# Performance work log

Measured on AMD Instinct MI355X. Metric: run time of the kernel, lower is better.

## Reference

```python
import jax, jax.numpy as jnp
import numpy as np

N_NODES = 50000
N_EDGES = 1600000
IN_FEAT = 48
OUT_FEAT = 48
NUM_RELS = 8


def setup_inputs() -> dict:
    key = jax.random.key(0)
    ks = jax.random.split(key, 9)
    # xavier-ish scale for relu gain
    s1 = float(np.sqrt(2.0) * np.sqrt(6.0 / (IN_FEAT + IN_FEAT)))
    s2 = float(np.sqrt(2.0) * np.sqrt(6.0 / (IN_FEAT + OUT_FEAT)))
    return {
        "inputs": jax.random.normal(ks[0], (N_NODES, IN_FEAT), dtype=jnp.float32),
        "norm": jax.random.uniform(ks[1], (N_EDGES, 1), dtype=jnp.float32),
        "weight1": jax.random.uniform(ks[2], (NUM_RELS, IN_FEAT, IN_FEAT), jnp.float32, -s1, s1),
        "weight2": jax.random.uniform(ks[3], (NUM_RELS, IN_FEAT, OUT_FEAT), jnp.float32, -s2, s2),
        "bias1": jax.random.normal(ks[4], (IN_FEAT,), dtype=jnp.float32) * 0.1,
        "bias2": jax.random.normal(ks[5], (OUT_FEAT,), dtype=jnp.float32) * 0.1,
        "src": jax.random.randint(ks[6], (N_EDGES,), 0, N_NODES, dtype=jnp.int64) if jax.config.jax_enable_x64 else jax.random.randint(ks[6], (N_EDGES,), 0, N_NODES).astype(jnp.int32),
        "dst": jax.random.randint(ks[7], (N_EDGES,), 0, N_NODES).astype(jnp.int32),
        "rel_type": jax.random.randint(ks[8], (N_EDGES,), 0, NUM_RELS).astype(jnp.int32),
    }


def reference(inputs, norm, weight1, weight2, bias1, bias2, src, dst, rel_type):
    # Message depends only on (src node, relation): precompute per (node, rel).
    # Stage 1: h1[n,r,:] = relu(h[n] @ W1[r] + b1)   -> [N, R, in]
    h1 = jax.nn.relu(jnp.einsum('ni,rij->nrj', inputs, weight1) + bias1)
    # Stage 2: h2[n,r,:] = h1[n,r] @ W2[r]           -> [N, R, out]
    h2 = jnp.einsum('nrj,rjo->nro', h1, weight2)
    # Per-edge gather + norm scaling                 -> [E, out]
    msg = h2[src, rel_type] * norm
    # Scatter-sum aggregation to destination nodes   -> [N, out]
    agg = jax.ops.segment_sum(msg, dst, num_segments=inputs.shape[0])
    # apply_func: bias2 + activation
    return jax.nn.relu(agg + bias2)
```

## Files before the change

kernel.cpp:

```cpp
#include <hip/hip_runtime.h>

#define NN 50000
#define EE 1600000
#define FF 48
#define RR 8
#define H2R 48
#define LSTR 72
#define NSEG 8
#define SCAP 16

#define WB 8
#define ZB 391
#define K1GRID (WB + ZB)

#define H2TILES 391
#define PB ((EE + 255) / 256)
#define K2GRID (H2TILES + PB)

typedef __attribute__((ext_vector_type(8))) short frag8;
typedef __attribute__((ext_vector_type(4))) float frag4f;
typedef __attribute__((ext_vector_type(4))) unsigned uint4v;

__device__ inline unsigned short bf16r(float f) {
    unsigned u = __float_as_uint(f);
    return (unsigned short)((u + 0x7FFFu + ((u >> 16) & 1u)) >> 16);
}
__device__ inline unsigned bf16pack2(float a, float b) {
    return (unsigned)bf16r(a) | ((unsigned)bf16r(b) << 16);
}
__device__ inline frag8 pack8(float4 a, float4 b) {
    union { frag8 f; unsigned u[4]; } r;
    r.u[0] = bf16pack2(a.x, a.y); r.u[1] = bf16pack2(a.z, a.w);
    r.u[2] = bf16pack2(b.x, b.y); r.u[3] = bf16pack2(b.z, b.w);
    return r.f;
}

__global__ __launch_bounds__(256) void pre_kernel(
    const float* __restrict__ W1, const float* __restrict__ W2,
    unsigned short* __restrict__ W1t, unsigned short* __restrict__ W2t,
    int* __restrict__ count)
{
    int b = blockIdx.x;
    if (b < WB) {
        int r = b;
        const float* w1 = W1 + (size_t)r * FF * FF;
        const float* w2 = W2 + (size_t)r * FF * FF;
        for (int idx = threadIdx.x; idx < 48 * 64; idx += 256) {
            int j = idx >> 6, k = idx & 63;
            W1t[(size_t)r * 48 * 64 + idx] = (k < FF) ? bf16r(w1[k * FF + j]) : (unsigned short)0;
            W2t[(size_t)r * 48 * 64 + idx] = (k < FF) ? bf16r(w2[k * FF + j]) : (unsigned short)0;
        }
        return;
    }
    int z = (b - WB) * 256 + threadIdx.x;
    if (z < 100000) ((int4*)count)[z] = make_int4(0, 0, 0, 0);
}

__global__ __launch_bounds__(256) void h2_place_kernel(
    const float* __restrict__ X, const unsigned short* __restrict__ W1t,
    const unsigned short* __restrict__ W2t, const float* __restrict__ B1,
    const int* __restrict__ srcv, const int* __restrict__ dstv,
    const int* __restrict__ relv, const float* __restrict__ norm,
    int* __restrict__ count, unsigned* __restrict__ payload,
    unsigned short* __restrict__ H2)
{
    __shared__ __align__(16) unsigned short h1s[128 * LSTR];
    __shared__ __align__(16) unsigned short h2s[128 * 96];
    int b = blockIdx.x;
    if (b >= H2TILES) {
        int e = (b - H2TILES) * 256 + threadIdx.x;
        if (e < EE) {
            int xcd;
            asm volatile("s_getreg_b32 %0, hwreg(HW_REG_XCC_ID)" : "=s"(xcd));
            xcd &= (NSEG - 1);
            int d = dstv[e];
            unsigned qn = (unsigned)(norm[e] * 8192.0f + 0.5f);
            if (qn > 8191u) qn = 8191u;
            unsigned rec = ((unsigned)(srcv[e] * 8 + relv[e]) << 13) | qn;
            int x = xcd;
            #pragma unroll 1
            for (int attempt = 0; attempt < NSEG; ++attempt) {
                int pos = atomicAdd(&count[x * NN + d], 1);
                if (pos < SCAP) {
                    payload[((size_t)x * NN + d) * SCAP + pos] = rec;
                    break;
                }
                x = (x + 1) & (NSEG - 1);
            }
        }
        return;
    }
    int tid  = threadIdx.x;
    int w    = tid >> 6, ln = tid & 63, q = ln >> 4, lq = ln & 15;
    int nb   = b * 128 + w * 32;

    unsigned short* myh1 = &h1s[(w * 32) * LSTR];
    unsigned short* myh2 = &h2s[w * 32 * 96];
    for (int i = ln; i < 32 * 12; i += 64) {
        int rr = i / 12, cs = i - rr * 12;
        *(unsigned*)&myh1[rr * LSTR + 48 + cs * 2] = 0;
    }

    int row0 = nb + lq;      if (row0 >= NN) row0 = NN - 1;
    int row1 = nb + 16 + lq; if (row1 >= NN) row1 = NN - 1;
    const float* x0 = X + (size_t)row0 * FF;
    const float* x1 = X + (size_t)row1 * FF;

    frag8 a00 = pack8(*(const float4*)(x0 + q * 8), *(const float4*)(x0 + q * 8 + 4));
    frag8 a10 = pack8(*(const float4*)(x1 + q * 8), *(const float4*)(x1 + q * 8 + 4));
    frag8 a01 = {0, 0, 0, 0, 0, 0, 0, 0};
    frag8 a11 = {0, 0, 0, 0, 0, 0, 0, 0};
    if (q < 2) {
        a01 = pack8(*(const float4*)(x0 + 32 + q * 8), *(const float4*)(x0 + 36 + q * 8));
        a11 = pack8(*(const float4*)(x1 + 32 + q * 8), *(const float4*)(x1 + 36 + q * 8));
    }

    float bcv[3] = {B1[lq], B1[16 + lq], B1[32 + lq]};

    #pragma unroll 1
    for (int kp = 0; kp < 4; ++kp) {
        #pragma unroll
        for (int p = 0; p < 2; ++p) {
            int r = (kp << 1) + p;
            const unsigned short* w1r = W1t + (size_t)r * 48 * 64;
            const unsigned short* w2r = W2t + (size_t)r * 48 * 64;

            #pragma unroll
            for (int t = 0; t < 3; ++t) {
                int col = t * 16 + lq;
                frag8 b0 = *(const frag8*)&w1r[(col << 6) + q * 8];
                frag8 b1 = *(const frag8*)&w1r[(col << 6) + 32 + q * 8];
                float bc = bcv[t];
                frag4f acc0 = {bc, bc, bc, bc};
                frag4f acc1 = {bc, bc, bc, bc};
                acc0 = __builtin_amdgcn_mfma_f32_16x16x32_bf16(a00, b0, acc0, 0, 0, 0);
                acc0 = __builtin_amdgcn_mfma_f32_16x16x32_bf16(a01, b1, acc0, 0, 0, 0);
                acc1 = __builtin_amdgcn_mfma_f32_16x16x32_bf16(a10, b0, acc1, 0, 0, 0);
                acc1 = __builtin_amdgcn_mfma_f32_16x16x32_bf16(a11, b1, acc1, 0, 0, 0);
                #pragma unroll
                for (int g = 0; g < 4; ++g) {
                    myh1[(q * 4 + g) * LSTR + col]      = bf16r(fmaxf(acc0[g], 0.0f));
                    myh1[(16 + q * 4 + g) * LSTR + col] = bf16r(fmaxf(acc1[g], 0.0f));
                }
            }

            const frag8 c00 = *(const frag8*)&myh1[lq * LSTR + q * 8];
            const frag8 c01 = *(const frag8*)&myh1[lq * LSTR + 32 + q * 8];
            const frag8 c10 = *(const frag8*)&myh1[(16 + lq) * LSTR + q * 8];
            const frag8 c11 = *(const frag8*)&myh1[(16 + lq) * LSTR + 32 + q * 8];

            #pragma unroll
            for (int t = 0; t < 3; ++t) {
                int col = t * 16 + lq;
                frag8 b0 = *(const frag8*)&w2r[(col << 6) + q * 8];
                frag8 b1 = *(const frag8*)&w2r[(col << 6) + 32 + q * 8];
                frag4f acc0 = {0.f, 0.f, 0.f, 0.f};
                frag4f acc1 = {0.f, 0.f, 0.f, 0.f};
                acc0 = __builtin_amdgcn_mfma_f32_16x16x32_bf16(c00, b0, acc0, 0, 0, 0);
                acc0 = __builtin_amdgcn_mfma_f32_16x16x32_bf16(c01, b1, acc0, 0, 0, 0);
                acc1 = __builtin_amdgcn_mfma_f32_16x16x32_bf16(c10, b0, acc1, 0, 0, 0);
                acc1 = __builtin_amdgcn_mfma_f32_16x16x32_bf16(c11, b1, acc1, 0, 0, 0);
                #pragma unroll
                for (int g = 0; g < 4; ++g) {
                    myh2[(q * 4 + g) * 96 + p * 48 + col]      = bf16r(acc0[g]);
                    myh2[(16 + q * 4 + g) * 96 + p * 48 + col] = bf16r(acc1[g]);
                }
            }
        }
        #pragma unroll
        for (int i6 = 0; i6 < 6; ++i6) {
            int fl    = i6 * 64 + ln;
            int row   = fl / 12;
            int piece = fl - row * 12;
            int n     = nb + row;
            if (n < NN) {
                uint4v v = *(const uint4v*)&myh2[fl * 8];
                __builtin_nontemporal_store(v,
                    (uint4v*)(H2 + ((size_t)n * RR + kp * 2) * H2R) + piece);
            }
        }
    }
}

__global__ __launch_bounds__(256) void gather_kernel(
    const unsigned short* __restrict__ H2, const unsigned* __restrict__ payload,
    const int* __restrict__ count, const float* __restrict__ B2,
    float* __restrict__ out)
{
    unsigned tid = blockIdx.x * 256u + threadIdx.x;
    unsigned n = tid / 12u;
    unsigned c = tid - n * 12u;
    if (n >= NN) return;

    int cx[NSEG];
    #pragma unroll
    for (int x = 0; x < NSEG; ++x) cx[x] = min(count[(size_t)x * NN + n], SCAP);
    int p1 = cx[0], p2 = p1 + cx[1], p3 = p2 + cx[2], p4 = p3 + cx[3];
    int p5 = p4 + cx[4], p6 = p5 + cx[5], p7 = p6 + cx[6];
    int total = p7 + cx[7];
    const unsigned* pl = payload + (size_t)n * SCAP;

    auto slot = [&](int idx) -> unsigned {
        int x, base;
        if (idx < p4) {
            if (idx < p2) { x = (idx < p1) ? 0 : 1; base = (idx < p1) ? 0 : p1; }
            else          { x = (idx < p3) ? 2 : 3; base = (idx < p3) ? p2 : p3; }
        } else {
            if (idx < p6) { x = (idx < p5) ? 4 : 5; base = (idx < p5) ? p4 : p5; }
            else          { x = (idx < p7) ? 6 : 7; base = (idx < p7) ? p6 : p7; }
        }
        return pl[(size_t)x * (NN * SCAP) + (idx - base)];
    };

    float a0 = 0.f, a1 = 0.f, a2 = 0.f, a3 = 0.f;
    int e = 0;
    for (; e + 8 <= total; e += 8) {
        unsigned p[8];
        #pragma unroll
        for (int k = 0; k < 8; ++k) p[k] = slot(e + k);
        uint2 v[8];
        #pragma unroll
        for (int k = 0; k < 8; ++k)
            v[k] = ((const uint2*)(H2 + (size_t)(p[k] >> 13) * H2R))[c];
        #pragma unroll
        for (int k = 0; k < 8; ++k) {
            float nm = (float)(p[k] & 8191u) * (1.0f / 8192.0f);
            a0 = fmaf(__uint_as_float(v[k].x << 16),         nm, a0);
            a1 = fmaf(__uint_as_float(v[k].x & 0xFFFF0000u), nm, a1);
            a2 = fmaf(__uint_as_float(v[k].y << 16),         nm, a2);
            a3 = fmaf(__uint_as_float(v[k].y & 0xFFFF0000u), nm, a3);
        }
    }
    for (; e < total; ++e) {
        unsigned p = slot(e);
        float nm = (float)(p & 8191u) * (1.0f / 8192.0f);
        uint2 v = ((const uint2*)(H2 + (size_t)(p >> 13) * H2R))[c];
        a0 = fmaf(__uint_as_float(v.x << 16),         nm, a0);
        a1 = fmaf(__uint_as_float(v.x & 0xFFFF0000u), nm, a1);
        a2 = fmaf(__uint_as_float(v.y << 16),         nm, a2);
        a3 = fmaf(__uint_as_float(v.y & 0xFFFF0000u), nm, a3);
    }
    float4 bbb = ((const float4*)B2)[c];
    ((float4*)out)[(size_t)n * 12u + c] = make_float4(
        fmaxf(a0 + bbb.x, 0.f), fmaxf(a1 + bbb.y, 0.f),
        fmaxf(a2 + bbb.z, 0.f), fmaxf(a3 + bbb.w, 0.f));
}

extern "C" void kernel_launch(void* const* d_in, const int* in_sizes, int n_in,
                              void* d_out, int out_size, void* d_ws, size_t ws_size,
                              hipStream_t stream) {
    const float* X   = (const float*)d_in[0];
    const float* nrm = (const float*)d_in[1];
    const float* W1  = (const float*)d_in[2];
    const float* W2  = (const float*)d_in[3];
    const float* B1  = (const float*)d_in[4];
    const float* B2  = (const float*)d_in[5];
    const int*   src = (const int*)d_in[6];
    const int*   dst = (const int*)d_in[7];
    const int*   rel = (const int*)d_in[8];
    float* out = (float*)d_out;

    unsigned short* H2      = (unsigned short*)d_ws;
    unsigned*       payload = (unsigned*)(H2 + (size_t)NN * RR * H2R);
    unsigned short* W1t     = (unsigned short*)(payload + (size_t)NN * NSEG * SCAP);
    unsigned short* W2t     = W1t + RR * 48 * 64;
    int*            count   = (int*)(W2t + RR * 48 * 64);

    pre_kernel<<<K1GRID, 256, 0, stream>>>(W1, W2, W1t, W2t, count);

    h2_place_kernel<<<K2GRID, 256, 0, stream>>>(
        X, W1t, W2t, B1, src, dst, rel, nrm, count, payload, H2);

    unsigned total = (unsigned)NN * 12u;
    gather_kernel<<<(total + 255) / 256, 256, 0, stream>>>(
        H2, payload, count, B2, out);
}
```

Measured before the change: 233.9 us.

## Switch H2 to relation-major layout and drop separate h2 shared buffer

```diff
diff --git a/kernel.cpp b/kernel.cpp
--- a/kernel.cpp
+++ b/kernel.cpp
@@ -20,6 +20,7 @@
 typedef __attribute__((ext_vector_type(8))) short frag8;
 typedef __attribute__((ext_vector_type(4))) float frag4f;
 typedef __attribute__((ext_vector_type(4))) unsigned uint4v;
+typedef __attribute__((ext_vector_type(4))) float float4v;
 
 __device__ inline unsigned short bf16r(float f) {
     unsigned u = __float_as_uint(f);
@@ -28,7 +29,7 @@
 __device__ inline unsigned bf16pack2(float a, float b) {
     return (unsigned)bf16r(a) | ((unsigned)bf16r(b) << 16);
 }
-__device__ inline frag8 pack8(float4 a, float4 b) {
+__device__ inline frag8 pack8(float4v a, float4v b) {
     union { frag8 f; unsigned u[4]; } r;
     r.u[0] = bf16pack2(a.x, a.y); r.u[1] = bf16pack2(a.z, a.w);
     r.u[2] = bf16pack2(b.x, b.y); r.u[3] = bf16pack2(b.z, b.w);
@@ -65,7 +66,6 @@
     unsigned short* __restrict__ H2)
 {
     __shared__ __align__(16) unsigned short h1s[128 * LSTR];
-    __shared__ __align__(16) unsigned short h2s[128 * 96];
     int b = blockIdx.x;
     if (b >= H2TILES) {
         int e = (b - H2TILES) * 256 + threadIdx.x;
@@ -73,10 +73,13 @@
             int xcd;
             asm volatile("s_getreg_b32 %0, hwreg(HW_REG_XCC_ID)" : "=s"(xcd));
             xcd &= (NSEG - 1);
-            int d = dstv[e];
-            unsigned qn = (unsigned)(norm[e] * 8192.0f + 0.5f);
+            int d  = __builtin_nontemporal_load(&dstv[e]);
+            int sv = __builtin_nontemporal_load(&srcv[e]);
+            int rv = __builtin_nontemporal_load(&relv[e]);
+            float nmv = __builtin_nontemporal_load(&norm[e]);
+            unsigned qn = (unsigned)(nmv * 8192.0f + 0.5f);
             if (qn > 8191u) qn = 8191u;
-            unsigned rec = ((unsigned)(srcv[e] * 8 + relv[e]) << 13) | qn;
+            unsigned rec = ((unsigned)(rv * NN + sv) << 13) | qn;
             int x = xcd;
             #pragma unroll 1
             for (int attempt = 0; attempt < NSEG; ++attempt) {
@@ -95,7 +98,6 @@
     int nb   = b * 128 + w * 32;
 
     unsigned short* myh1 = &h1s[(w * 32) * LSTR];
-    unsigned short* myh2 = &h2s[w * 32 * 96];
     for (int i = ln; i < 32 * 12; i += 64) {
         int rr = i / 12, cs = i - rr * 12;
         *(unsigned*)&myh1[rr * LSTR + 48 + cs * 2] = 0;
@@ -103,81 +105,80 @@
 
     int row0 = nb + lq;      if (row0 >= NN) row0 = NN - 1;
     int row1 = nb + 16 + lq; if (row1 >= NN) row1 = NN - 1;
-    const float* x0 = X + (size_t)row0 * FF;
-    const float* x1 = X + (size_t)row1 * FF;
-
-    frag8 a00 = pack8(*(const float4*)(x0 + q * 8), *(const float4*)(x0 + q * 8 + 4));
-    frag8 a10 = pack8(*(const float4*)(x1 + q * 8), *(const float4*)(x1 + q * 8 + 4));
+    const float4v* x0 = (const float4v*)(X + (size_t)row0 * FF);
+    const float4v* x1 = (const float4v*)(X + (size_t)row1 * FF);
+
+    frag8 a00 = pack8(__builtin_nontemporal_load(x0 + q * 2),
+                      __builtin_nontemporal_load(x0 + q * 2 + 1));
+    frag8 a10 = pack8(__builtin_nontemporal_load(x1 + q * 2),
+                      __builtin_nontemporal_load(x1 + q * 2 + 1));
     frag8 a01 = {0, 0, 0, 0, 0, 0, 0, 0};
     frag8 a11 = {0, 0, 0, 0, 0, 0, 0, 0};
     if (q < 2) {
-        a01 = pack8(*(const float4*)(x0 + 32 + q * 8), *(const float4*)(x0 + 36 + q * 8));
-        a11 = pack8(*(const float4*)(x1 + 32 + q * 8), *(const float4*)(x1 + 36 + q * 8));
+        a01 = pack8(__builtin_nontemporal_load(x0 + 8 + q * 2),
+                    __builtin_nontemporal_load(x0 + 9 + q * 2));
+        a11 = pack8(__builtin_nontemporal_load(x1 + 8 + q * 2),
+                    __builtin_nontemporal_load(x1 + 9 + q * 2));
     }
 
     float bcv[3] = {B1[lq], B1[16 + lq], B1[32 + lq]};
 
     #pragma unroll 1
-    for (int kp = 0; kp < 4; ++kp) {
-        #pragma unroll
-        for (int p = 0; p < 2; ++p) {
-            int r = (kp << 1) + p;
-            const unsigned short* w1r = W1t + (size_t)r * 48 * 64;
-            const unsigned short* w2r = W2t + (size_t)r * 48 * 64;
-
+    for (int r = 0; r < RR; ++r) {
+        const unsigned short* w1r = W1t + (size_t)r * 48 * 64;
+        const unsigned short* w2r = W2t + (size_t)r * 48 * 64;
+
+        #pragma unroll
+        for (int t = 0; t < 3; ++t) {
+            int col = t * 16 + lq;
+            frag8 b0 = *(const frag8*)&w1r[(col << 6) + q * 8];
+            frag8 b1 = *(const frag8*)&w1r[(col << 6) + 32 + q * 8];
+            float bc = bcv[t];
+            frag4f acc0 = {bc, bc, bc, bc};
+            frag4f acc1 = {bc, bc, bc, bc};
+            acc0 = __builtin_amdgcn_mfma_f32_16x16x32_bf16(a00, b0, acc0, 0, 0, 0);
+            acc0 = __builtin_amdgcn_mfma_f32_16x16x32_bf16(a01, b1, acc0, 0, 0, 0);
+            acc1 = __builtin_amdgcn_mfma_f32_16x16x32_bf16(a10, b0, acc1, 0, 0, 0);
+            acc1 = __builtin_amdgcn_mfma_f32_16x16x32_bf16(a11, b1, acc1, 0, 0, 0);
             #pragma unroll
-            for (int t = 0; t < 3; ++t) {
-                int col = t * 16 + lq;
-                frag8 b0 = *(const frag8*)&w1r[(col << 6) + q * 8];
-                frag8 b1 = *(const frag8*)&w1r[(col << 6) + 32 + q * 8];
-                float bc = bcv[t];
-                frag4f acc0 = {bc, bc, bc, bc};
-                frag4f acc1 = {bc, bc, bc, bc};
-                acc0 = __builtin_amdgcn_mfma_f32_16x16x32_bf16(a00, b0, acc0, 0, 0, 0);
-                acc0 = __builtin_amdgcn_mfma_f32_16x16x32_bf16(a01, b1, acc0, 0, 0, 0);
-                acc1 = __builtin_amdgcn_mfma_f32_16x16x32_bf16(a10, b0, acc1, 0, 0, 0);
-                acc1 = __builtin_amdgcn_mfma_f32_16x16x32_bf16(a11, b1, acc1, 0, 0, 0);
-                #pragma unroll
-                for (int g = 0; g < 4; ++g) {
-                    myh1[(q * 4 + g) * LSTR + col]      = bf16r(fmaxf(acc0[g], 0.0f));
-                    myh1[(16 + q * 4 + g) * LSTR + col] = bf16r(fmaxf(acc1[g], 0.0f));
-                }
+            for (int g = 0; g < 4; ++g) {
+                myh1[(q * 4 + g) * LSTR + col]      = bf16r(fmaxf(acc0[g], 0.0f));
+                myh1[(16 + q * 4 + g) * LSTR + col] = bf16r(fmaxf(acc1[g], 0.0f));
             }
-
-            const frag8 c00 = *(const frag8*)&myh1[lq * LSTR + q * 8];
-            const frag8 c01 = *(const frag8*)&myh1[lq * LSTR + 32 + q * 8];
-            const frag8 c10 = *(const frag8*)&myh1[(16 + lq) * LSTR + q * 8];
-            const frag8 c11 = *(const frag8*)&myh1[(16 + lq) * LSTR + 32 + q * 8];
-
+        }
+
+        const frag8 c00 = *(const frag8*)&myh1[lq * LSTR + q * 8];
+        const frag8 c01 = *(const frag8*)&myh1[lq * LSTR + 32 + q * 8];
+        const frag8 c10 = *(const frag8*)&myh1[(16 + lq) * LSTR + q * 8];
+        const frag8 c11 = *(const frag8*)&myh1[(16 + lq) * LSTR + 32 + q * 8];
+
+        #pragma unroll
+        for (int t = 0; t < 3; ++t) {
+            int col = t * 16 + lq;
+            frag8 b0 = *(const frag8*)&w2r[(col << 6) + q * 8];
+            frag8 b1 = *(const frag8*)&w2r[(col << 6) + 32 + q * 8];
+            frag4f acc0 = {0.f, 0.f, 0.f, 0.f};
+            frag4f acc1 = {0.f, 0.f, 0.f, 0.f};
+            acc0 = __builtin_amdgcn_mfma_f32_16x16x32_bf16(c00, b0, acc0, 0, 0, 0);
+            acc0 = __builtin_amdgcn_mfma_f32_16x16x32_bf16(c01, b1, acc0, 0, 0, 0);
+            acc1 = __builtin_amdgcn_mfma_f32_16x16x32_bf16(c10, b0, acc1, 0, 0, 0);
+            acc1 = __builtin_amdgcn_mfma_f32_16x16x32_bf16(c11, b1, acc1, 0, 0, 0);
             #pragma unroll
-            for (int t = 0; t < 3; ++t) {
-                int col = t * 16 + lq;
-                frag8 b0 = *(const frag8*)&w2r[(col << 6) + q * 8];
-                frag8 b1 = *(const frag8*)&w2r[(col << 6) + 32 + q * 8];
-                frag4f acc0 = {0.f, 0.f, 0.f, 0.f};
-                frag4f acc1 = {0.f, 0.f, 0.f, 0.f};
-                acc0 = __builtin_amdgcn_mfma_f32_16x16x32_bf16(c00, b0, acc0, 0, 0, 0);
-                acc0 = __builtin_amdgcn_mfma_f32_16x16x32_bf16(c01, b1, acc0, 0, 0, 0);
-                acc1 = __builtin_amdgcn_mfma_f32_16x16x32_bf16(c10, b0, acc1, 0, 0, 0);
-                acc1 = __builtin_amdgcn_mfma_f32_16x16x32_bf16(c11, b1, acc1, 0, 0, 0);
-                #pragma unroll
-                for (int g = 0; g < 4; ++g) {
-                    myh2[(q * 4 + g) * 96 + p * 48 + col]      = bf16r(acc0[g]);
-                    myh2[(16 + q * 4 + g) * 96 + p * 48 + col] = bf16r(acc1[g]);
-                }
+            for (int g = 0; g < 4; ++g) {
+                myh1[(q * 4 + g) * LSTR + col]      = bf16r(acc0[g]);
+                myh1[(16 + q * 4 + g) * LSTR + col] = bf16r(acc1[g]);
             }
         }
-        #pragma unroll
-        for (int i6 = 0; i6 < 6; ++i6) {
-            int fl    = i6 * 64 + ln;
-            int row   = fl / 12;
-            int piece = fl - row * 12;
+
+        unsigned short* dst = H2 + ((size_t)r * NN + nb) * H2R;
+        #pragma unroll
+        for (int i3 = 0; i3 < 3; ++i3) {
+            int fl    = i3 * 64 + ln;
+            int row   = fl / 6, piece = fl - row * 6;
             int n     = nb + row;
-            if (n < NN) {
-                uint4v v = *(const uint4v*)&myh2[fl * 8];
-                __builtin_nontemporal_store(v,
-                    (uint4v*)(H2 + ((size_t)n * RR + kp * 2) * H2R) + piece);
-            }
+            if (n < NN)
+                *(uint4v*)(dst + fl * 8) =
+                    *(const uint4v*)&myh1[row * LSTR + piece * 8];
         }
     }
 }
```

Measured after the change: 221.8 us. 1.05x faster.
